# Optimization experiments

Hardware: AMD Instinct MI355X
Metric: run time of the kernel (lower is better)

The kernel has to match this reference:

```python
import jax, jax.numpy as jnp
import numpy as np

N_TOTAL = 4_000_000   # raw decoded candidates
K = 4096              # candidates after confidence threshold (NMS input)
IMG_W, IMG_H = 1088.0, 608.0  # JDE input resolution
NMS_THRESH = 0.6


def setup_inputs() -> dict:
    key = jax.random.key(0)
    k1, k2, k3, k4, k5, k6 = jax.random.split(key, 6)
    # build valid boxes: x1<x2, y1<y2, inside image-ish
    cx = jax.random.uniform(k1, (N_TOTAL,)) * IMG_W
    cy = jax.random.uniform(k2, (N_TOTAL,)) * IMG_H
    w = jax.random.uniform(k3, (N_TOTAL,)) * 128.0 + 4.0
    h = jax.random.uniform(k4, (N_TOTAL,)) * 128.0 + 4.0
    scores = jax.random.uniform(k5, (N_TOTAL,))
    yolo_boxes_scores = jnp.stack(
        [cx - w * 0.5, cy - h * 0.5, cx + w * 0.5, cy + h * 0.5, scores], axis=1
    ).astype(jnp.float32)  # [N_TOTAL, 5] = x1,y1,x2,y2,score
    boxes_idx = jax.random.randint(k6, (K,), 0, N_TOTAL)  # [K]
    return {"yolo_boxes_scores": yolo_boxes_scores, "boxes_idx": boxes_idx}


def _pairwise_iou(x1, y1, x2, y2):
    # +1 pixel convention, matching the reference numpy nms()
    areas = (x2 - x1 + 1.0) * (y2 - y1 + 1.0)
    xx1 = jnp.maximum(x1[:, None], x1[None, :])
    yy1 = jnp.maximum(y1[:, None], y1[None, :])
    xx2 = jnp.minimum(x2[:, None], x2[None, :])
    yy2 = jnp.minimum(y2[:, None], y2[None, :])
    w = jnp.maximum(0.0, xx2 - xx1 + 1.0)
    h = jnp.maximum(0.0, yy2 - yy1 + 1.0)
    inter = w * h
    union = areas[:, None] + areas[None, :] - inter
    return inter / union  # [K, K]


def reference(yolo_boxes_scores, boxes_idx):
    # gather candidates passing confidence threshold (decode output)
    gathered = yolo_boxes_scores[boxes_idx]          # [K, 5] x1,y1,x2,y2,score
    boxes = gathered[:, :4]
    scores = gathered[:, 4]

    # sort by score descending (greedy NMS order)
    order = jnp.argsort(-scores)                     # [K]
    sb = boxes[order]
    ss = scores[order]

    iou = _pairwise_iou(sb[:, 0], sb[:, 1], sb[:, 2], sb[:, 3])  # [K, K]
    idx = jnp.arange(K)

    def body(i, supp):
        # if box i survives, suppress all later boxes with IoU >= thresh
        row = jnp.where(supp[i], jnp.zeros((K,), iou.dtype), iou[i])
        new = (idx > i) & (row >= NMS_THRESH)
        return supp | new

    suppressed = jax.lax.fori_loop(0, K, body, jnp.zeros((K,), bool))
    keep = ~suppressed                               # [K] in sorted order

    # bbox_pred rows: [label, score, x1, y1, x2, y2]; num_classes=1 -> label 0
    label = jnp.zeros((K, 1), jnp.float32)
    bbox_pred = jnp.concatenate([label, ss[:, None], sb], axis=1)
    bbox_pred = bbox_pred * keep[:, None].astype(bbox_pred.dtype)  # zero suppressed rows (fixed shape)
    bbox_num = keep.sum().astype(jnp.int32)
    nms_keep_idx = jnp.where(keep, order, -1).astype(jnp.int32)
    return bbox_pred, bbox_num, nms_keep_idx
```

## Files before the change

kernel.cpp:

```cpp
#include <hip/hip_runtime.h>
#include <cstdint>
#include <cstddef>

#define KBOX 4096
#define NMS_THRESH 0.6f

typedef unsigned long long u64;

static constexpr size_t WS_SB   = 0;
static constexpr size_t WS_AREA = 65536;
static constexpr size_t WS_SS   = 81920;
static constexpr size_t WS_ORD  = 98304;
static constexpr size_t WS_KEYS = 114688;
static constexpr size_t WS_MASK = 147456;

__device__ __forceinline__ void gload_lds16(const void* g, void* l) {
    __builtin_amdgcn_global_load_lds(
        (const __attribute__((address_space(1))) void*)g,
        (__attribute__((address_space(3))) void*)l, 16, 0, 0);
}

__global__ __launch_bounds__(256) void k_keys(const float* __restrict__ yolo,
                                              const int* __restrict__ bidx,
                                              u64* __restrict__ keys) {
    int p = blockIdx.x * 256 + threadIdx.x;
    size_t idx = (size_t)(unsigned)bidx[p];
    float s = yolo[idx * 5 + 4];
    keys[p] = ((u64)__float_as_uint(s) << 32)
            | (u64)(0xFFFFFFFFu - (unsigned)p);
}

__global__ __launch_bounds__(256) void k_rank(const u64* __restrict__ keys,
                                              const float* __restrict__ yolo,
                                              const int* __restrict__ bidx,
                                              float4* __restrict__ sb,
                                              float* __restrict__ area,
                                              float* __restrict__ ss,
                                              int* __restrict__ sord) {
    #pragma clang fp contract(off)
    int gid = blockIdx.x * 256 + threadIdx.x;
    int p = gid >> 6;
    int lane = gid & 63;

    u64 kp = keys[p];
    int cnt = 0;
    for (int k = 0; k < 64; ++k) {
        u64 kq = keys[k * 64 + lane];
        cnt += __popcll(__ballot(kq > kp));
    }

    if (lane == 0) {
        int r = cnt;
        size_t idx = (size_t)(unsigned)bidx[p];
        float x1 = yolo[idx * 5 + 0];
        float y1 = yolo[idx * 5 + 1];
        float x2 = yolo[idx * 5 + 2];
        float y2 = yolo[idx * 5 + 3];
        float s  = __uint_as_float((unsigned)(kp >> 32));
        sb[r] = make_float4(x1, y1, x2, y2);
        area[r] = (x2 - x1 + 1.0f) * (y2 - y1 + 1.0f);
        ss[r] = s;
        sord[r] = p;
    }
}

__global__ __launch_bounds__(256) void k_mask(const float4* __restrict__ sb,
                                              const float* __restrict__ area,
                                              u64* __restrict__ mask) {
    #pragma clang fp contract(off)
    int gid = blockIdx.x * 256 + threadIdx.x;
    int i = gid >> 6;
    int lane = gid & 63;

    float4 bi = sb[i];
    float ai = area[i];
    u64 myword = 0ull;

    for (int k = 0; k < 64; ++k) {
        int j = k * 64 + lane;
        float4 bj = sb[j];
        float xx1 = fmaxf(bi.x, bj.x);
        float yy1 = fmaxf(bi.y, bj.y);
        float xx2 = fminf(bi.z, bj.z);
        float yy2 = fminf(bi.w, bj.w);
        float w = fmaxf(0.0f, xx2 - xx1 + 1.0f);
        float h = fmaxf(0.0f, yy2 - yy1 + 1.0f);
        float inter = w * h;
        float uni = (ai + area[j]) - inter;
        float iou = inter / uni;
        bool pred = (iou >= NMS_THRESH) && (j > i);
        u64 bal = __ballot(pred);
        if (k == lane) myword = bal;
    }
    mask[(size_t)i * 64 + lane] = myword;
}

__global__ __launch_bounds__(256) void k_reduce_out(const u64* __restrict__ mask,
                                                    const float4* __restrict__ sb,
                                                    const float* __restrict__ ss,
                                                    const int* __restrict__ sord,
                                                    float* __restrict__ out) {
    __shared__ u64 stage[2][64 * 64];
    __shared__ u64 keep_lds[64];
    const int tid = threadIdx.x;
    const int wid = tid >> 6;
    const int lane = tid & 63;

    {
        const char* src = (const char*)mask;
        char* dst = (char*)stage[0];
        for (int b = wid; b < 32; b += 4)
            gload_lds16(src + b * 1024 + lane * 16, dst + b * 1024);
    }
    __syncthreads();

    u64 remv = 0ull;

    for (int c = 0; c < 64; ++c) {
        if (wid != 0) {
            if (c + 1 < 64) {
                const char* src = (const char*)(mask + (size_t)(c + 1) * 4096);
                char* dst = (char*)stage[(c + 1) & 1];
                for (int b = wid - 1; b < 32; b += 3)
                    gload_lds16(src + b * 1024 + lane * 16, dst + b * 1024);
            }
        } else {
            const u64* buf = stage[c & 1];

            u64 bcu = buf[(lane << 6) + c];
            u64 sup = __shfl(remv, c);
            u64 kept = 0ull;
            #pragma unroll
            for (int u = 0; u < 64; ++u) {
                u64 bc_u = __shfl(bcu, u);
                u64 sbit = (sup >> u) & 1ull;
                kept |= (sbit ^ 1ull) << u;
                sup  |= sbit ? 0ull : bc_u;
            }

            u64 acc = 0ull;
            #pragma unroll
            for (int u = 0; u < 64; ++u) {
                u64 m = buf[(u << 6) | lane];
                acc |= m & (0ull - ((kept >> u) & 1ull));
            }
            remv |= acc;
        }
        __syncthreads();
    }

    if (tid < 64) {
        u64 kw = ~remv;
        keep_lds[tid] = kw;
        int cnt = __popcll(kw);
        for (int off = 32; off > 0; off >>= 1) cnt += __shfl_down(cnt, off);
        if (tid == 0) out[(size_t)KBOX * 6] = (float)cnt;
    }
    __syncthreads();

    for (int p = tid; p < KBOX; p += 256) {
        bool keep = (keep_lds[p >> 6] >> (p & 63)) & 1ull;
        float4 b = sb[p];
        float s = ss[p];
        int o = sord[p];

        float* row = out + (size_t)p * 6;
        row[0] = 0.0f;
        row[1] = keep ? s   : 0.0f;
        row[2] = keep ? b.x : 0.0f;
        row[3] = keep ? b.y : 0.0f;
        row[4] = keep ? b.z : 0.0f;
        row[5] = keep ? b.w : 0.0f;

        out[(size_t)KBOX * 6 + 1 + p] = keep ? (float)o : -1.0f;
    }
}

extern "C" void kernel_launch(void* const* d_in, const int* in_sizes, int n_in,
                              void* d_out, int out_size, void* d_ws, size_t ws_size,
                              hipStream_t stream) {
    const float* yolo = (const float*)d_in[0];
    const int* bidx   = (const int*)d_in[1];
    float* out = (float*)d_out;

    char* ws = (char*)d_ws;
    float4* sb  = (float4*)(ws + WS_SB);
    float* area = (float*)(ws + WS_AREA);
    float* ss   = (float*)(ws + WS_SS);
    int* sord   = (int*)(ws + WS_ORD);
    u64* keys   = (u64*)(ws + WS_KEYS);
    u64* mask   = (u64*)(ws + WS_MASK);

    k_keys<<<KBOX / 256, 256, 0, stream>>>(yolo, bidx, keys);
    k_rank<<<(KBOX * 64) / 256, 256, 0, stream>>>(keys, yolo, bidx, sb, area, ss, sord);
    k_mask<<<(KBOX * 64) / 256, 256, 0, stream>>>(sb, area, mask);
    k_reduce_out<<<1, 256, 0, stream>>>(mask, sb, ss, sord, out);
}
```

Baseline: 341.5 us.

## Split NMS reduce across all four waves with sparse kept-box scan

The serial NMS reduction now has all four waves both prefetch the next mask chunk and OR-reduce suppression rows, each wave covering 16 rows. Before, one wave did all the compute while three only loaded. The per-chunk greedy scan replaces the fixed 64-step shuffle loop with a loop that only visits surviving boxes, using ctz and a skip mask. Cross-wave suppression state passes through a small double-buffered LDS handoff that is read before each barrier. This shortens the serial critical path in exchange for extra LDS traffic and data-dependent loop lengths.

```diff
diff --git a/kernel.cpp b/kernel.cpp
--- a/kernel.cpp
+++ b/kernel.cpp
@@ -101,6 +101,7 @@
                                                     const int* __restrict__ sord,
                                                     float* __restrict__ out) {
     __shared__ u64 stage[2][64 * 64];
+    __shared__ u64 hand[2][4];
     __shared__ u64 keep_lds[64];
     const int tid = threadIdx.x;
     const int wid = tid >> 6;
@@ -112,47 +113,51 @@
         for (int b = wid; b < 32; b += 4)
             gload_lds16(src + b * 1024 + lane * 16, dst + b * 1024);
     }
+    if (tid < 8) hand[tid >> 2][tid & 3] = 0ull;
     __syncthreads();
 
-    u64 remv = 0ull;
+    u64 partial = 0ull;
 
     for (int c = 0; c < 64; ++c) {
-        if (wid != 0) {
-            if (c + 1 < 64) {
-                const char* src = (const char*)(mask + (size_t)(c + 1) * 4096);
-                char* dst = (char*)stage[(c + 1) & 1];
-                for (int b = wid - 1; b < 32; b += 3)
-                    gload_lds16(src + b * 1024 + lane * 16, dst + b * 1024);
-            }
-        } else {
-            const u64* buf = stage[c & 1];
-
-            u64 bcu = buf[(lane << 6) + c];
-            u64 sup = __shfl(remv, c);
-            u64 kept = 0ull;
-            #pragma unroll
-            for (int u = 0; u < 64; ++u) {
-                u64 bc_u = __shfl(bcu, u);
-                u64 sbit = (sup >> u) & 1ull;
-                kept |= (sbit ^ 1ull) << u;
-                sup  |= sbit ? 0ull : bc_u;
-            }
-
-            u64 acc = 0ull;
-            #pragma unroll
-            for (int u = 0; u < 64; ++u) {
-                u64 m = buf[(u << 6) | lane];
-                acc |= m & (0ull - ((kept >> u) & 1ull));
-            }
-            remv |= acc;
+        if (c + 1 < 64) {
+            const char* src = (const char*)(mask + (size_t)(c + 1) * 4096);
+            char* dst = (char*)stage[(c + 1) & 1];
+            for (int b = wid; b < 32; b += 4)
+                gload_lds16(src + b * 1024 + lane * 16, dst + b * 1024);
         }
+
+        const u64* buf = stage[c & 1];
+
+        u64 sup0 = hand[c & 1][0] | hand[c & 1][1] | hand[c & 1][2] | hand[c & 1][3];
+
+        u64 bcu = buf[(lane << 6) + c];
+
+        u64 undec = ~sup0;
+        u64 kept = 0ull;
+        while (undec) {
+            int u0 = __builtin_ctzll(undec);
+            u64 supset = __shfl(bcu, u0);
+            kept |= 1ull << u0;
+            undec &= ~(supset | (1ull << u0));
+        }
+
+        u64 acc = 0ull;
+        #pragma unroll
+        for (int k = 0; k < 16; ++k) {
+            int u = (wid << 4) + k;
+            u64 m = buf[(u << 6) | lane];
+            acc |= m & (0ull - ((kept >> u) & 1ull));
+        }
+        partial |= acc;
+
+        if (wid == 0 && lane == 0) keep_lds[c] = kept;
+        if (lane == c + 1) hand[(c + 1) & 1][wid] = partial;
+
         __syncthreads();
     }
 
     if (tid < 64) {
-        u64 kw = ~remv;
-        keep_lds[tid] = kw;
-        int cnt = __popcll(kw);
+        int cnt = __popcll(keep_lds[tid]);
         for (int off = 32; off > 0; off >>= 1) cnt += __shfl_down(cnt, off);
         if (tid == 0) out[(size_t)KBOX * 6] = (float)cnt;
     }
```

Result: slower. 441.1 us (+29.2%).
